# Performance work log

Measured on AMD Instinct MI355X. Metric: run time of the kernel, lower is better.

Reference implementation:

```python
import jax, jax.numpy as jnp
import numpy as np

S = 4096      # keystrokes
H = 32        # hidden_dim / d_model
NH = 8        # nhead
HD = H // NH  # head dim = 4
FF = 2048     # torch TransformerEncoderLayer default dim_feedforward
NL = 6        # num_layers
EPS = 1e-5


def setup_inputs() -> dict:
    key = jax.random.key(0)
    ks = jax.random.split(key, 20)
    sc = 0.02
    ts = jnp.sort(jax.random.uniform(ks[0], (S,), minval=0.0, maxval=2.49e7))
    feats = jax.random.normal(ks[1], (S, 2), dtype=jnp.float32)
    data = jnp.concatenate([ts[:, None], feats], axis=1)  # [S, 3]
    return {
        "data": data,
        "lin_w": jax.random.normal(ks[2], (H, 2)) * sc,
        "lin_b": jnp.zeros((H,)),
        "qkv_w": jax.random.normal(ks[3], (NL, 3 * H, H)) * sc,
        "qkv_b": jnp.zeros((NL, 3 * H)),
        "out_w": jax.random.normal(ks[4], (NL, H, H)) * sc,
        "out_b": jnp.zeros((NL, H)),
        "ln1_g": jnp.ones((NL, H)),
        "ln1_b": jnp.zeros((NL, H)),
        "ff1_w": jax.random.normal(ks[5], (NL, FF, H)) * sc,
        "ff1_b": jnp.zeros((NL, FF)),
        "ff2_w": jax.random.normal(ks[6], (NL, H, FF)) * sc,
        "ff2_b": jnp.zeros((NL, H)),
        "ln2_g": jnp.ones((NL, H)),
        "ln2_b": jnp.zeros((NL, H)),
        "cls_w": jax.random.normal(ks[7], (1, H)) * sc,
        "cls_b": jnp.zeros((1,)),
    }


def _ln(x, g, b):
    m = x.mean(-1, keepdims=True)
    v = ((x - m) ** 2).mean(-1, keepdims=True)
    return (x - m) / jnp.sqrt(v + EPS) * g + b


def reference(data, lin_w, lin_b, qkv_w, qkv_b, out_w, out_b,
              ln1_g, ln1_b, ff1_w, ff1_b, ff2_w, ff2_b,
              ln2_g, ln2_b, cls_w, cls_b):
    # per-keystroke Linear+ReLU, vectorized over the sequence
    x = jax.nn.relu(data[:, 1:] @ lin_w.T + lin_b)            # [S, H]
    # sinusoidal time encoding at index timestamp//100
    ts_idx = (data[:, 0] / 100.0).astype(jnp.int32)            # [S]
    div = jnp.exp(jnp.arange(0, H, 2, dtype=jnp.float32) * (-np.log(10000.0) / H))
    ang = ts_idx[:, None].astype(jnp.float32) * div            # [S, H/2]
    pe = jnp.stack([jnp.sin(ang), jnp.cos(ang)], axis=-1).reshape(S, H)
    x = x + pe
    # prepend CLS token of -1.0 -> seq len S+1
    x = jnp.concatenate([jnp.full((1, H), -1.0, dtype=x.dtype), x], axis=0)
    L = S + 1
    for i in range(NL):  # post-LN encoder layers (torch defaults, eval/no-dropout)
        qkv = x @ qkv_w[i].T + qkv_b[i]                        # [L, 3H]
        q, k, v = jnp.split(qkv, 3, axis=-1)
        q = q.reshape(L, NH, HD)
        k = k.reshape(L, NH, HD)
        v = v.reshape(L, NH, HD)
        scores = jnp.einsum('qhd,khd->hqk', q, k) / np.sqrt(HD)
        attn = jax.nn.softmax(scores, axis=-1)                 # [NH, L, L]
        o = jnp.einsum('hqk,khd->qhd', attn, v).reshape(L, H)
        o = o @ out_w[i].T + out_b[i]
        x = _ln(x + o, ln1_g[i], ln1_b[i])
        f = jax.nn.relu(x @ ff1_w[i].T + ff1_b[i]) @ ff2_w[i].T + ff2_b[i]
        x = _ln(x + f, ln2_g[i], ln2_b[i])
    cls_out = x[0]                                             # [H]
    return jax.nn.sigmoid(cls_out @ cls_w.T + cls_b)           # [1]
```

## Files before the change

kernel.cpp:

```cpp
#include <hip/hip_runtime.h>
#include <hip/hip_bf16.h>
#include <math.h>

#define SEQ 4096
#define LL  4097
#define HDIM 32
#define FFD 2048
#define NLAYER 6
#define EPSLN 1e-5f
#define NCHUNK 16
#define KPAD 4128
#define QROWS 4352
#define RB2 16

#if __has_builtin(__builtin_amdgcn_exp2f)
#define EXP2 __builtin_amdgcn_exp2f
#else
#define EXP2 exp2f
#endif

#define QSCALE 0.7213475204444817f

typedef short bf16x8 __attribute__((ext_vector_type(8)));
typedef short bf16x4 __attribute__((ext_vector_type(4)));
typedef float f32x4 __attribute__((ext_vector_type(4)));

__device__ __forceinline__ unsigned short f2b(float f) {
  unsigned int b = __float_as_uint(f);
  b += 0x7FFFu + ((b >> 16) & 1u);
  return (unsigned short)(b >> 16);
}

__device__ __forceinline__ unsigned int pk_bf16(float a, float b) {
  __hip_bfloat162 h = __float22bfloat162_rn(make_float2(a, b));
  return *(unsigned int*)&h;
}

__device__ __forceinline__ f32x4 mfma_qk(bf16x4 a, bf16x4 b, f32x4 c) {
#if __has_builtin(__builtin_amdgcn_mfma_f32_16x16x16bf16_1k)
  return __builtin_amdgcn_mfma_f32_16x16x16bf16_1k(a, b, c, 0, 0, 0);
#else
  bf16x8 a8 = {a[0], a[1], a[2], a[3], 0, 0, 0, 0};
  bf16x8 b8 = {b[0], b[1], b[2], b[3], 0, 0, 0, 0};
  return __builtin_amdgcn_mfma_f32_16x16x32_bf16(a8, b8, c, 0, 0, 0);
#endif
}


__device__ __forceinline__ void qkv_wave(float y, int row, bool ok, int lane,
    const float* __restrict__ qw, const float* __restrict__ qb,
    unsigned short* __restrict__ Qb, unsigned short* __restrict__ KB4,
    unsigned short* __restrict__ VB5) {
  int ch = lane & 31;
  float xv[32];
#pragma unroll
  for (int k = 0; k < 32; ++k) xv[k] = __shfl(y, (lane & 32) + k, 64);
#pragma unroll
  for (int t3 = 0; t3 < 3; ++t3) {
    int cc = t3 * 32 + ch;
    const float4* wr = (const float4*)(qw + (size_t)cc * 32);
    float acc = qb[cc];
#pragma unroll
    for (int k8 = 0; k8 < 8; ++k8) {
      float4 wv = wr[k8];
      acc = fmaf(xv[4 * k8 + 0], wv.x, acc);
      acc = fmaf(xv[4 * k8 + 1], wv.y, acc);
      acc = fmaf(xv[4 * k8 + 2], wv.z, acc);
      acc = fmaf(xv[4 * k8 + 3], wv.w, acc);
    }
    if (ok) {
      int h = ch >> 2;
      if (t3 == 0) {
        Qb[(size_t)row * 32 + ch] = f2b(QSCALE * acc);
      } else if (t3 == 1) {
        KB4[((size_t)h * KPAD + row) * 4 + (ch & 3)] = f2b(acc);
      } else {
        int w = row & 31;
        int pos = ((w & 15) << 1) | (w >> 4);
        VB5[((size_t)h * 5 + (ch & 3)) * KPAD + (row & ~31) + pos] = f2b(acc);
      }
    }
  }
}

__global__ __launch_bounds__(256) void k_init(const float* __restrict__ data,
    const float* __restrict__ lin_w, const float* __restrict__ lin_b,
    const float* __restrict__ qkv_w, const float* __restrict__ qkv_b,
    const float* __restrict__ ff1_w, const float* __restrict__ ff2_w,
    float* __restrict__ X, unsigned short* __restrict__ Qb,
    unsigned short* __restrict__ KB4, unsigned short* __restrict__ VB5,
    unsigned short* __restrict__ W1B, unsigned short* __restrict__ W2B) {
  int gid = blockIdx.x * 256 + threadIdx.x;
  int gsz = gridDim.x * 256;
  const int NW = NLAYER * FFD * 32;
  for (int i = gid; i < NW; i += gsz) {
    W1B[i] = f2b(ff1_w[i]);
    W2B[i] = f2b(ff2_w[i]);
  }
  for (int i = gid; i < (QROWS - LL) * 32; i += gsz)
    Qb[(size_t)LL * 32 + i] = 0;
  for (int i = gid; i < 8 * (KPAD - LL) * 4; i += gsz) {
    int hh = i / ((KPAD - LL) * 4);
    int rem = i % ((KPAD - LL) * 4);
    KB4[((size_t)hh * KPAD + LL) * 4 + rem] = 0;
  }
  for (int i = gid; i < 8 * 5 * KPAD; i += gsz) {
    int col = i % KPAD;
    int dd = (i / KPAD) % 5;
    if (dd == 4) {
      int key = (col & ~31) + ((col & 1) << 4) + ((col & 31) >> 1);
      VB5[i] = (key <= 4096) ? 0x3F80 : 0;
    } else if (col > 4096) {
      VB5[i] = 0;
    }
  }
  int wave = threadIdx.x >> 6, lane = threadIdx.x & 63;
  int r = lane >> 5, ch = lane & 31;
  unsigned wgid = blockIdx.x * 4 + wave;
  for (unsigned it = wgid; it < 2049; it += gridDim.x * 4) {
    int row = it * 2 + r;
    bool ok = row < LL;
    float val = 0.f;
    if (ok) {
      if (row == 0) {
        val = -1.0f;
      } else {
        int s = row - 1;
        float ts = data[s * 3 + 0];
        float f0 = data[s * 3 + 1];
        float f1 = data[s * 3 + 2];
        float lin = f0 * lin_w[ch * 2 + 0] + f1 * lin_w[ch * 2 + 1] + lin_b[ch];
        lin = fmaxf(lin, 0.0f);
        int tsi = (int)(ts / 100.0f);
        int j = ch >> 1;
        float aj = (float)(2 * j) * (float)(-0.28782313662425575);
        float divj = (float)exp((double)aj);
        float ang = (float)tsi * divj;
        float pe = (ch & 1) ? cosf(ang) : sinf(ang);
        val = lin + pe;
      }
      X[(size_t)row * HDIM + ch] = val;
    }
    qkv_wave(val, row, ok, lane, qkv_w, qkv_b, Qb, KB4, VB5);
  }
}

__global__ __launch_bounds__(256, 4) void k_attn(
    const unsigned short* __restrict__ Qb, const unsigned short* __restrict__ KB4,
    const unsigned short* __restrict__ VB5, float* __restrict__ LP,
    float4* __restrict__ AP4) {
  int tid = threadIdx.x;
  int wave = tid >> 6, lane = tid & 63;
  int l16 = lane & 15, quad = lane >> 4;
  int h = blockIdx.y, c = blockIdx.z;
  int qs = blockIdx.x * 4 + wave;
  if (qs >= 65) return;
  int q0 = qs * 64;
  int kb0 = c * 256;
  int nkb = (c == NCHUNK - 1) ? 9 : 8;

  const unsigned short* KBh = KB4 + (size_t)h * KPAD * 4;
  const unsigned short* VBh = VB5 + (size_t)h * 5 * KPAD;
  const bool kl = (quad == (h & 3));
  const bool vl = (l16 < 5);
  const int qcol0 = (h >> 2) * 16 + quad * 4;

  bf16x4 aq[4];
#pragma unroll
  for (int t = 0; t < 4; ++t)
    aq[t] = *(const bf16x4*)&Qb[(size_t)(q0 + t * 16 + l16) * 32 + qcol0];

  const bf16x4 zb4 = {0, 0, 0, 0};
  const bf16x8 zb8 = {0, 0, 0, 0, 0, 0, 0, 0};
  f32x4 acc0[4], acc1[4];
#pragma unroll
  for (int t = 0; t < 4; ++t) {
    acc0[t] = (f32x4){0.f, 0.f, 0.f, 0.f};
    acc1[t] = (f32x4){0.f, 0.f, 0.f, 0.f};
  }

  auto step = [&](int k0, f32x4* acc) {
    bf16x4 bk0 = kl ? *(const bf16x4*)&KBh[(size_t)(k0 + l16) * 4] : zb4;
    bf16x4 bk1 = kl ? *(const bf16x4*)&KBh[(size_t)(k0 + 16 + l16) * 4] : zb4;
    bf16x8 bv = vl ? *(const bf16x8*)&VBh[(size_t)l16 * KPAD + k0 + quad * 8]
                   : zb8;
    f32x4 z = {0.f, 0.f, 0.f, 0.f};
    unsigned pf[4][4];
#pragma unroll
    for (int t = 0; t < 4; ++t) {
      f32x4 s0 = mfma_qk(bk0, aq[t], z);
      f32x4 s1 = mfma_qk(bk1, aq[t], z);
#pragma unroll
      for (int reg = 0; reg < 4; ++reg)
        pf[t][reg] = pk_bf16(EXP2(s0[reg]), EXP2(s1[reg]));
    }
#pragma unroll
    for (int t = 0; t < 4; ++t) {
      bf16x8 pb = *(const bf16x8*)&pf[t][0];
      acc[t] = __builtin_amdgcn_mfma_f32_16x16x32_bf16(bv, pb, acc[t], 0, 0, 0);
    }
  };

  int kb = 0;
  for (; kb + 2 <= nkb; kb += 2) {
    step(kb0 + kb * 32, acc0);
    step(kb0 + (kb + 1) * 32, acc1);
  }
  if (kb < nkb) step(kb0 + kb * 32, acc0);

#pragma unroll
  for (int t = 0; t < 4; ++t) {
    f32x4 a = acc0[t] + acc1[t];
    int q = q0 + t * 16 + l16;
    if (q < LL) {
      if (quad == 0) {
        AP4[((size_t)c * LL + q) * 8 + h] = make_float4(a[0], a[1], a[2], a[3]);
      } else if (quad == 1) {
        LP[((size_t)c * LL + q) * 8 + h] = a[0];
      }
    }
  }
}

__global__ __launch_bounds__(512, 4) void k_ffnF(const float* __restrict__ LP,
    const float* __restrict__ APf, float* __restrict__ X,
    const float* __restrict__ ow, const float* __restrict__ ob,
    const float* __restrict__ g1, const float* __restrict__ b1ln,
    const unsigned short* __restrict__ w1b, const float* __restrict__ fb1,
    const unsigned short* __restrict__ w2b, const float* __restrict__ fb2,
    const float* __restrict__ g2, const float* __restrict__ b2ln,
    const float* __restrict__ qw, const float* __restrict__ qb,
    unsigned short* __restrict__ Qb, unsigned short* __restrict__ KB4,
    unsigned short* __restrict__ VB5, int do_qkv,
    const float* __restrict__ cw, const float* __restrict__ cb,
    float* __restrict__ out) {
  __shared__ unsigned short Xa[RB2][32];
  __shared__ float Y1[RB2][32];
  __shared__ unsigned short Fsb[8][16 * 136];
  __shared__ float Pr[8][RB2 * 33];
  int tid = threadIdx.x;
  int wave = tid >> 6, lane = tid & 63;
  int l16 = lane & 15, quad = lane >> 4;
  int r = lane >> 5, ch = lane & 31;
  int r0 = blockIdx.x * RB2;

  {
    int rl = wave * 2 + r;
    int row = r0 + rl;
    bool ok = row < LL;
    int hh = ch >> 2;
    float L = 0.f, A = 0.f;
    if (ok) {
#pragma unroll
      for (int c = 0; c < NCHUNK; ++c) {
        A += APf[((size_t)c * LL + row) * 32 + ch];
        L += LP[((size_t)c * LL + row) * 8 + hh];
      }
    }
    float os = ok ? A / L : 0.f;
    float acc = 0.f;
    const float4* owr = (const float4*)(ow + (size_t)ch * 32);
#pragma unroll
    for (int k8 = 0; k8 < 8; ++k8) {
      float4 wv = owr[k8];
      acc = fmaf(__shfl(os, (lane & 32) + 4 * k8 + 0, 64), wv.x, acc);
      acc = fmaf(__shfl(os, (lane & 32) + 4 * k8 + 1, 64), wv.y, acc);
      acc = fmaf(__shfl(os, (lane & 32) + 4 * k8 + 2, 64), wv.z, acc);
      acc = fmaf(__shfl(os, (lane & 32) + 4 * k8 + 3, 64), wv.w, acc);
    }
    float val = ok ? (X[(size_t)row * HDIM + ch] + acc + ob[ch]) : 0.f;
    float mean = val;
#pragma unroll
    for (int off = 16; off > 0; off >>= 1) mean += __shfl_xor(mean, off, 32);
    mean *= (1.f / 32.f);
    float d2 = val - mean;
    float var = d2 * d2;
#pragma unroll
    for (int off = 16; off > 0; off >>= 1) var += __shfl_xor(var, off, 32);
    var *= (1.f / 32.f);
    float y = d2 / sqrtf(var + EPSLN) * g1[ch] + b1ln[ch];
    Y1[rl][ch] = y;
    Xa[rl][ch] = ok ? f2b(y) : 0;
  }
  __syncthreads();

  bf16x8 a1 = *(const bf16x8*)&Xa[l16][quad * 8];
  f32x4 acc2[2] = {{0.f, 0.f, 0.f, 0.f}, {0.f, 0.f, 0.f, 0.f}};
  int fs0 = wave * 256;
#pragma unroll
  for (int sg = 0; sg < 2; ++sg) {
    int f0 = fs0 + sg * 128;
    f32x4 c1[8];
#pragma unroll
    for (int t = 0; t < 8; ++t) {
      bf16x8 b =
          *(const bf16x8*)&w1b[(size_t)(f0 + t * 16 + l16) * 32 + quad * 8];
      f32x4 z = {0.f, 0.f, 0.f, 0.f};
      c1[t] = __builtin_amdgcn_mfma_f32_16x16x32_bf16(a1, b, z, 0, 0, 0);
    }
#pragma unroll
    for (int t = 0; t < 8; ++t) {
      float bb = fb1[f0 + t * 16 + l16];
#pragma unroll
      for (int reg = 0; reg < 4; ++reg) {
        float v = fmaxf(c1[t][reg] + bb, 0.f);
        Fsb[wave][(quad * 4 + reg) * 136 + t * 16 + l16] = f2b(v);
      }
    }
#pragma unroll
    for (int kt = 0; kt < 4; ++kt) {
      bf16x8 a2 = *(const bf16x8*)&Fsb[wave][l16 * 136 + kt * 32 + quad * 8];
#pragma unroll
      for (int u = 0; u < 2; ++u) {
        bf16x8 b = *(const bf16x8*)&w2b[(size_t)(u * 16 + l16) * FFD + f0 +
                                        kt * 32 + quad * 8];
        acc2[u] =
            __builtin_amdgcn_mfma_f32_16x16x32_bf16(a2, b, acc2[u], 0, 0, 0);
      }
    }
  }
#pragma unroll
  for (int u = 0; u < 2; ++u)
#pragma unroll
    for (int reg = 0; reg < 4; ++reg)
      Pr[wave][(quad * 4 + reg) * 33 + u * 16 + l16] = acc2[u][reg];
  __syncthreads();

  {
    int rl = wave * 2 + r;
    int row = r0 + rl;
    bool ok = row < LL;
    float s = 0.f;
#pragma unroll
    for (int w = 0; w < 8; ++w) s += Pr[w][rl * 33 + ch];
    float val = ok ? (Y1[rl][ch] + s + fb2[ch]) : 0.f;
    float mean = val;
#pragma unroll
    for (int off = 16; off > 0; off >>= 1) mean += __shfl_xor(mean, off, 32);
    mean *= (1.f / 32.f);
    float d2 = val - mean;
    float var = d2 * d2;
#pragma unroll
    for (int off = 16; off > 0; off >>= 1) var += __shfl_xor(var, off, 32);
    var *= (1.f / 32.f);
    float y = d2 / sqrtf(var + EPSLN) * g2[ch] + b2ln[ch];
    if (ok) X[(size_t)row * HDIM + ch] = y;
    if (do_qkv) {
      qkv_wave(y, row, ok, lane, qw, qb, Qb, KB4, VB5);
    } else if (blockIdx.x == 0 && wave == 0 && r == 0) {
      float t = y * cw[ch];
#pragma unroll
      for (int off = 16; off > 0; off >>= 1) t += __shfl_xor(t, off, 32);
      if (ch == 0) out[0] = 1.f / (1.f + expf(-(t + cb[0])));
    }
  }
}

extern "C" void kernel_launch(void* const* d_in, const int* in_sizes, int n_in,
                              void* d_out, int out_size, void* d_ws,
                              size_t ws_size, hipStream_t stream) {
  const float* data  = (const float*)d_in[0];
  const float* lin_w = (const float*)d_in[1];
  const float* lin_b = (const float*)d_in[2];
  const float* qkv_w = (const float*)d_in[3];
  const float* qkv_b = (const float*)d_in[4];
  const float* out_w = (const float*)d_in[5];
  const float* out_b = (const float*)d_in[6];
  const float* ln1_g = (const float*)d_in[7];
  const float* ln1_b = (const float*)d_in[8];
  const float* ff1_w = (const float*)d_in[9];
  const float* ff1_b = (const float*)d_in[10];
  const float* ff2_w = (const float*)d_in[11];
  const float* ff2_b = (const float*)d_in[12];
  const float* ln2_g = (const float*)d_in[13];
  const float* ln2_b = (const float*)d_in[14];
  const float* cls_w = (const float*)d_in[15];
  const float* cls_b = (const float*)d_in[16];

  char* wsb = (char*)d_ws;
  float* X = (float*)wsb;
  unsigned short* Qb  = (unsigned short*)(X + (size_t)LL * 32);
  unsigned short* KB4 = Qb + (size_t)QROWS * 32;
  unsigned short* VB5 = KB4 + (size_t)8 * KPAD * 4;
  unsigned short* W1B = VB5 + (size_t)8 * 5 * KPAD;
  unsigned short* W2B = W1B + (size_t)NLAYER * FFD * 32;
  float4* AP = (float4*)(((size_t)(W2B + (size_t)NLAYER * FFD * 32) + 15) &
                         ~(size_t)15);
  float* LP = (float*)(AP + (size_t)NCHUNK * LL * 8);

  k_init<<<1024, 256, 0, stream>>>(data, lin_w, lin_b, qkv_w, qkv_b,
                                   ff1_w, ff2_w, X, Qb, KB4, VB5, W1B, W2B);
  for (int l = 0; l < NLAYER; ++l) {
    k_attn<<<dim3(17, 8, NCHUNK), 256, 0, stream>>>(Qb, KB4, VB5, LP, AP);
    int nl = l + 1;
    int do_qkv = (nl < NLAYER) ? 1 : 0;
    const float* qw = qkv_w + (size_t)(do_qkv ? nl : 0) * 96 * 32;
    const float* qb = qkv_b + (size_t)(do_qkv ? nl : 0) * 96;
    k_ffnF<<<(LL + RB2 - 1) / RB2, 512, 0, stream>>>(
        LP, (const float*)AP, X,
        out_w + (size_t)l * 32 * 32, out_b + (size_t)l * 32,
        ln1_g + (size_t)l * 32, ln1_b + (size_t)l * 32,
        W1B + (size_t)l * FFD * 32, ff1_b + (size_t)l * FFD,
        W2B + (size_t)l * FFD * 32, ff2_b + (size_t)l * 32,
        ln2_g + (size_t)l * 32, ln2_b + (size_t)l * 32,
        qw, qb, Qb, KB4, VB5, do_qkv, cls_w, cls_b, (float*)d_out);
  }
}
```

Measured before the change: 400.6 us.

## Compute only the CLS row in the final encoder layer

The output depends only on the CLS token, so the last layer no longer runs full attention and FFN over all 4097 rows. A single-block kernel computes CLS attention over all keys, then the out-projection, LN, FFN, LN and the classifier for that one row. This drops roughly one sixth of the attention and FFN work, but the new kernel is a serial single-block pass over 4097 keys and the full fp32 FFN weights, so it could itself take noticeable time.

```diff
diff --git a/kernel.cpp b/kernel.cpp
--- a/kernel.cpp
+++ b/kernel.cpp
@@ -29,6 +29,11 @@
   unsigned int b = __float_as_uint(f);
   b += 0x7FFFu + ((b >> 16) & 1u);
   return (unsigned short)(b >> 16);
+}
+
+__device__ __forceinline__ float b2f(unsigned short u) {
+  unsigned int b = ((unsigned int)u) << 16;
+  return __uint_as_float(b);
 }
 
 __device__ __forceinline__ unsigned int pk_bf16(float a, float b) {
@@ -231,9 +236,7 @@
     const float* __restrict__ g2, const float* __restrict__ b2ln,
     const float* __restrict__ qw, const float* __restrict__ qb,
     unsigned short* __restrict__ Qb, unsigned short* __restrict__ KB4,
-    unsigned short* __restrict__ VB5, int do_qkv,
-    const float* __restrict__ cw, const float* __restrict__ cb,
-    float* __restrict__ out) {
+    unsigned short* __restrict__ VB5) {
   __shared__ unsigned short Xa[RB2][32];
   __shared__ float Y1[RB2][32];
   __shared__ unsigned short Fsb[8][16 * 136];
@@ -345,14 +348,114 @@
     var *= (1.f / 32.f);
     float y = d2 / sqrtf(var + EPSLN) * g2[ch] + b2ln[ch];
     if (ok) X[(size_t)row * HDIM + ch] = y;
-    if (do_qkv) {
-      qkv_wave(y, row, ok, lane, qw, qb, Qb, KB4, VB5);
-    } else if (blockIdx.x == 0 && wave == 0 && r == 0) {
-      float t = y * cw[ch];
-#pragma unroll
-      for (int off = 16; off > 0; off >>= 1) t += __shfl_xor(t, off, 32);
-      if (ch == 0) out[0] = 1.f / (1.f + expf(-(t + cb[0])));
-    }
+    qkv_wave(y, row, ok, lane, qw, qb, Qb, KB4, VB5);
+  }
+}
+
+__global__ __launch_bounds__(256) void k_last(
+    const unsigned short* __restrict__ Qb, const unsigned short* __restrict__ KB4,
+    const unsigned short* __restrict__ VB5, const float* __restrict__ X,
+    const float* __restrict__ ow, const float* __restrict__ ob,
+    const float* __restrict__ g1, const float* __restrict__ b1ln,
+    const float* __restrict__ w1, const float* __restrict__ fb1,
+    const float* __restrict__ w2, const float* __restrict__ fb2,
+    const float* __restrict__ g2, const float* __restrict__ b2ln,
+    const float* __restrict__ cw, const float* __restrict__ cb,
+    float* __restrict__ out) {
+  __shared__ float os_sh[32];
+  __shared__ float y1_sh[32];
+  __shared__ float f_sh[FFD];
+  __shared__ float red[8][32];
+  int tid = threadIdx.x;
+  int h = tid >> 5, l32 = tid & 31;
+
+  float q[4];
+#pragma unroll
+  for (int d = 0; d < 4; ++d) q[d] = b2f(Qb[h * 4 + d]);
+  float num[4] = {0.f, 0.f, 0.f, 0.f};
+  float den = 0.f;
+#pragma unroll 2
+  for (int k = l32; k < LL; k += 32) {
+    bf16x4 kr = *(const bf16x4*)&KB4[((size_t)h * KPAD + k) * 4];
+    float s = 0.f;
+#pragma unroll
+    for (int d = 0; d < 4; ++d)
+      s = fmaf(q[d], b2f((unsigned short)kr[d]), s);
+    float p = EXP2(s);
+    int w = k & 31;
+    int pos = (k & ~31) + (((w & 15) << 1) | (w >> 4));
+#pragma unroll
+    for (int d = 0; d < 4; ++d)
+      num[d] = fmaf(p, b2f(VB5[((size_t)h * 5 + d) * KPAD + pos]), num[d]);
+    den += p;
+  }
+#pragma unroll
+  for (int off = 16; off > 0; off >>= 1) {
+#pragma unroll
+    for (int d = 0; d < 4; ++d) num[d] += __shfl_xor(num[d], off, 32);
+    den += __shfl_xor(den, off, 32);
+  }
+  if (l32 < 4) os_sh[h * 4 + l32] = num[l32] / den;
+  __syncthreads();
+
+  if (tid < 32) {
+    int ch = tid;
+    float acc = 0.f;
+#pragma unroll
+    for (int k = 0; k < 32; ++k) acc = fmaf(os_sh[k], ow[ch * 32 + k], acc);
+    float val = X[ch] + acc + ob[ch];
+    float mean = val;
+#pragma unroll
+    for (int off = 16; off > 0; off >>= 1) mean += __shfl_xor(mean, off, 32);
+    mean *= (1.f / 32.f);
+    float d2 = val - mean;
+    float var = d2 * d2;
+#pragma unroll
+    for (int off = 16; off > 0; off >>= 1) var += __shfl_xor(var, off, 32);
+    var *= (1.f / 32.f);
+    y1_sh[ch] = d2 / sqrtf(var + EPSLN) * g1[ch] + b1ln[ch];
+  }
+  __syncthreads();
+
+  for (int i = tid; i < FFD; i += 256) {
+    const float* wr = w1 + (size_t)i * 32;
+    float acc = fb1[i];
+#pragma unroll
+    for (int j = 0; j < 32; ++j) acc = fmaf(y1_sh[j], wr[j], acc);
+    f_sh[i] = fmaxf(acc, 0.f);
+  }
+  __syncthreads();
+
+  {
+    float acc = 0.f;
+    const float* wr = w2 + (size_t)l32 * FFD + h * 256;
+    const float* fr = &f_sh[h * 256];
+#pragma unroll 8
+    for (int j = 0; j < 256; ++j) acc = fmaf(fr[j], wr[j], acc);
+    red[h][l32] = acc;
+  }
+  __syncthreads();
+
+  if (tid < 32) {
+    int ch = tid;
+    float s = 0.f;
+#pragma unroll
+    for (int sg = 0; sg < 8; ++sg) s += red[sg][ch];
+    float val = y1_sh[ch] + s + fb2[ch];
+    float mean = val;
+#pragma unroll
+    for (int off = 16; off > 0; off >>= 1) mean += __shfl_xor(mean, off, 32);
+    mean *= (1.f / 32.f);
+    float d2 = val - mean;
+    float var = d2 * d2;
+#pragma unroll
+    for (int off = 16; off > 0; off >>= 1) var += __shfl_xor(var, off, 32);
+    var *= (1.f / 32.f);
+    float y = d2 / sqrtf(var + EPSLN) * g2[ch] + b2ln[ch];
+    float t = y * cw[ch];
+#pragma unroll
+    for (int off = 16; off > 0; off >>= 1) t += __shfl_xor(t, off, 32);
+    if (ch == 0) out[0] = 1.f / (1.f + expf(-(t + cb[0])));
   }
 }
 
@@ -390,12 +493,10 @@
 
   k_init<<<1024, 256, 0, stream>>>(data, lin_w, lin_b, qkv_w, qkv_b,
                                    ff1_w, ff2_w, X, Qb, KB4, VB5, W1B, W2B);
-  for (int l = 0; l < NLAYER; ++l) {
+  for (int l = 0; l < NLAYER - 1; ++l) {
     k_attn<<<dim3(17, 8, NCHUNK), 256, 0, stream>>>(Qb, KB4, VB5, LP, AP);
-    int nl = l + 1;
-    int do_qkv = (nl < NLAYER) ? 1 : 0;
-    const float* qw = qkv_w + (size_t)(do_qkv ? nl : 0) * 96 * 32;
-    const float* qb = qkv_b + (size_t)(do_qkv ? nl : 0) * 96;
+    const float* qw = qkv_w + (size_t)(l + 1) * 96 * 32;
+    const float* qb = qkv_b + (size_t)(l + 1) * 96;
     k_ffnF<<<(LL + RB2 - 1) / RB2, 512, 0, stream>>>(
         LP, (const float*)AP, X,
         out_w + (size_t)l * 32 * 32, out_b + (size_t)l * 32,
@@ -403,6 +504,17 @@
         W1B + (size_t)l * FFD * 32, ff1_b + (size_t)l * FFD,
         W2B + (size_t)l * FFD * 32, ff2_b + (size_t)l * 32,
         ln2_g + (size_t)l * 32, ln2_b + (size_t)l * 32,
-        qw, qb, Qb, KB4, VB5, do_qkv, cls_w, cls_b, (float*)d_out);
-  }
-}
+        qw, qb, Qb, KB4, VB5);
+  }
+  {
+    const int l = NLAYER - 1;
+    k_last<<<1, 256, 0, stream>>>(
+        Qb, KB4, VB5, X,
+        out_w + (size_t)l * 32 * 32, out_b + (size_t)l * 32,
+        ln1_g + (size_t)l * 32, ln1_b + (size_t)l * 32,
+        ff1_w + (size_t)l * FFD * 32, ff1_b + (size_t)l * FFD,
+        ff2_w + (size_t)l * 32 * FFD, ff2_b + (size_t)l * 32,
+        ln2_g + (size_t)l * 32, ln2_b + (size_t)l * 32,
+        cls_w, cls_b, (float*)d_out);
+  }
+}
```

New measurement: 405.2 us. About the same (+1.1%).
